# Kernel tuning notes

Hardware: AMD Instinct MI355X
Metric: run time of the kernel (lower is better)

Reference implementation:

```python
import jax, jax.numpy as jnp
import numpy as np

IOU_THRESHOLD = 0.5
EPS = 1e-7


def _make_boxes(key, n, h, w):
    k1, k2, k3, k4 = jax.random.split(key, 4)
    x1 = jax.random.uniform(k1, (n,)) * (w - 120.0)
    y1 = jax.random.uniform(k2, (n,)) * (h - 120.0)
    x2 = x1 + 20.0 + jax.random.uniform(k3, (n,)) * 100.0
    y2 = y1 + 20.0 + jax.random.uniform(k4, (n,)) * 100.0
    return jnp.stack([x1, y1, x2, y2], axis=1).astype(jnp.float32)


def setup_inputs() -> dict:
    key = jax.random.key(0)
    kd, ka, km, kt = jax.random.split(key, 4)
    N, K, H, W, MH, MW = 512, 100, 800, 800, 28, 28
    detections = _make_boxes(kd, N, H, W)[None]          # (1, N, 4) pixel coords
    annotations = _make_boxes(ka, K, H, W)[None]          # (1, K, 4) pixel coords
    masks = jax.random.uniform(km, (1, N, MH, MW, K), dtype=jnp.float32)
    masks_target = jax.random.uniform(kt, (1, K, H, W), dtype=jnp.float32)
    return {"detections": detections, "masks": masks,
            "annotations": annotations, "masks_target": masks_target}


def _overlap(a, b):
    # a: (N,4), b: (K,4) -> IoU (N,K)
    area = (b[:, 2] - b[:, 0]) * (b[:, 3] - b[:, 1])                      # (K,)
    iw = jnp.minimum(a[:, 2:3], b[None, :, 2]) - jnp.maximum(a[:, 0:1], b[None, :, 0])
    ih = jnp.minimum(a[:, 3:4], b[None, :, 3]) - jnp.maximum(a[:, 1:2], b[None, :, 1])
    iw = jnp.maximum(iw, 0.0)
    ih = jnp.maximum(ih, 0.0)
    inter = iw * ih
    ua = ((a[:, 2] - a[:, 0]) * (a[:, 3] - a[:, 1]))[:, None] + area[None, :] - inter
    return inter / jnp.maximum(ua, EPS)


def _crop_and_resize(images, boxes, box_ind, crop_size):
    # TF crop_and_resize (bilinear, extrapolation_value=0) on single-channel images.
    # images: (B, H, W); boxes: (M,4) normalized [y1,x1,y2,x2]; box_ind: (M,) int
    H, W = images.shape[1], images.shape[2]
    ch, cw = crop_size
    y1, x1, y2, x2 = boxes[:, 0], boxes[:, 1], boxes[:, 2], boxes[:, 3]
    gy = jnp.arange(ch, dtype=boxes.dtype) / (ch - 1)
    gx = jnp.arange(cw, dtype=boxes.dtype) / (cw - 1)
    in_y = (y1[:, None] + (y2 - y1)[:, None] * gy) * (H - 1)  # (M, ch)
    in_x = (x1[:, None] + (x2 - x1)[:, None] * gx) * (W - 1)  # (M, cw)
    valid_y = (in_y >= 0) & (in_y <= H - 1)
    valid_x = (in_x >= 0) & (in_x <= W - 1)
    y0 = jnp.floor(in_y)
    x0 = jnp.floor(in_x)
    yf = (in_y - y0)[:, :, None]
    xf = (in_x - x0)[:, None, :]
    y0i = jnp.clip(y0.astype(jnp.int32), 0, H - 1)
    y1i = jnp.clip(y0i + 1, 0, H - 1)
    x0i = jnp.clip(x0.astype(jnp.int32), 0, W - 1)
    x1i = jnp.clip(x0i + 1, 0, W - 1)
    b = box_ind[:, None, None]
    v00 = images[b, y0i[:, :, None], x0i[:, None, :]]
    v01 = images[b, y0i[:, :, None], x1i[:, None, :]]
    v10 = images[b, y1i[:, :, None], x0i[:, None, :]]
    v11 = images[b, y1i[:, :, None], x1i[:, None, :]]
    top = v00 + (v01 - v00) * xf
    bot = v10 + (v11 - v10) * xf
    out = top + (bot - top) * yf                                # (M, ch, cw)
    return jnp.where(valid_y[:, :, None] & valid_x[:, None, :], out, 0.0)


def reference(detections, masks, annotations, masks_target):
    d = detections[0]          # (N, 4)
    m = masks[0]               # (N, mh, mw, C)
    a = annotations[0]         # (K, 4)
    mt = masks_target[0]       # (K, H, W)
    N, mh, mw = m.shape[0], m.shape[1], m.shape[2]
    H, W = mt.shape[1], mt.shape[2]

    iou = _overlap(d, a)                               # (N, K)
    argmax_inds = jnp.argmax(iou, axis=1)              # (N,)
    max_iou = jnp.max(iou, axis=1)                     # (N,)
    valid = (max_iou >= IOU_THRESHOLD).astype(d.dtype)  # mask instead of dynamic gather

    x1, y1, x2, y2 = d[:, 0], d[:, 1], d[:, 2], d[:, 3]
    boxes = jnp.stack([y1 / H, x1 / W, y2 / H, x2 / W], axis=1)  # (N,4) normalized

    target = _crop_and_resize(mt, boxes, argmax_inds, (mh, mw))  # (N, mh, mw)
    # select the mask channel matching the assigned annotation index
    m_sel = jnp.take_along_axis(m, argmax_inds[:, None, None, None], axis=3)[..., 0]

    diff = jnp.abs(m_sel - target) * valid[:, None, None]
    n_sel = jnp.sum(valid)
    divisor = jnp.maximum(n_sel * mh * mw, 1.0)
    return jnp.sum(diff) / divisor
```

## Files before the change

### kernel.cpp

```cpp
#include <hip/hip_runtime.h>
#include <math.h>

#define N_DET 512
#define K_ANN 100
#define MH    28
#define MW    28
#define NPIX  (MH * MW)
#define IMH   800
#define IMW   800
#define IOU_THRESH 0.5f
#define EPS_F 1e-7f


__global__ __launch_bounds__(256) void maskloss_fused(
    const float* __restrict__ det,
    const float* __restrict__ masks,
    const float* __restrict__ ann,
    const float* __restrict__ mt,
    int*   __restrict__ wsi,
    float* __restrict__ wsf,
    float* __restrict__ out)
{
    __shared__ float s_iou;
    __shared__ int   s_k;
    __shared__ float wsum[4];

    const int n   = blockIdx.x;
    const int tid = threadIdx.x;

    const float dx1 = det[n * 4 + 0];
    const float dy1 = det[n * 4 + 1];
    const float dx2 = det[n * 4 + 2];
    const float dy2 = det[n * 4 + 3];

    if (tid < 64) {
        const float darea = (dx2 - dx1) * (dy2 - dy1);
        float best = -1.0f;
        int   bidx = 0x7FFFFFFF;
        for (int k = tid; k < K_ANN; k += 64) {
            const float ax1 = ann[k * 4 + 0];
            const float ay1 = ann[k * 4 + 1];
            const float ax2 = ann[k * 4 + 2];
            const float ay2 = ann[k * 4 + 3];
            const float area_k = (ax2 - ax1) * (ay2 - ay1);
            float iw = fminf(dx2, ax2) - fmaxf(dx1, ax1);
            float ih = fminf(dy2, ay2) - fmaxf(dy1, ay1);
            iw = fmaxf(iw, 0.0f);
            ih = fmaxf(ih, 0.0f);
            const float inter = iw * ih;
            const float ua = darea + area_k - inter;
            const float iou = inter / fmaxf(ua, EPS_F);
            if (iou > best) { best = iou; bidx = k; }
        }
        for (int m = 32; m > 0; m >>= 1) {
            const float ov = __shfl_xor(best, m);
            const int   oi = __shfl_xor(bidx, m);
            if (ov > best || (ov == best && oi < bidx)) { best = ov; bidx = oi; }
        }
        if (tid == 0) { s_iou = best; s_k = bidx; }
    }
    __syncthreads();

    const bool valid = (s_iou >= IOU_THRESH);
    const int  k     = s_k;

    if (valid) {
        const float by1 = dy1 / (float)IMH;
        const float bx1 = dx1 / (float)IMW;
        const float by2 = dy2 / (float)IMH;
        const float bx2 = dx2 / (float)IMW;

        const float* __restrict__ img = mt    + (size_t)k * (IMH * IMW);
        const float* __restrict__ msk = masks + (size_t)n * (NPIX * K_ANN) + k;

        auto px = [&](int p) -> float {
            const int i = p / MW;
            const int j = p - i * MW;
            const float gy = (float)i * (1.0f / (float)(MH - 1));
            const float gx = (float)j * (1.0f / (float)(MW - 1));
            const float in_y = (by1 + (by2 - by1) * gy) * (float)(IMH - 1);
            const float in_x = (bx1 + (bx2 - bx1) * gx) * (float)(IMW - 1);
            const bool vy = (in_y >= 0.0f) && (in_y <= (float)(IMH - 1));
            const bool vx = (in_x >= 0.0f) && (in_x <= (float)(IMW - 1));
            const float y0f = floorf(in_y);
            const float x0f = floorf(in_x);
            const float yf = in_y - y0f;
            const float xf = in_x - x0f;
            int y0i = (int)y0f;
            int x0i = (int)x0f;
            y0i = min(max(y0i, 0), IMH - 1);
            x0i = min(max(x0i, 0), IMW - 1);
            const int y1i = min(y0i + 1, IMH - 1);
            const int x1i = min(x0i + 1, IMW - 1);

            const float msel = msk[(size_t)p * K_ANN];
            const float v00 = img[y0i * IMW + x0i];
            const float v01 = img[y0i * IMW + x1i];
            const float v10 = img[y1i * IMW + x0i];
            const float v11 = img[y1i * IMW + x1i];
            const float top = v00 + (v01 - v00) * xf;
            const float bot = v10 + (v11 - v10) * xf;
            float outv = top + (bot - top) * yf;
            outv = (vy && vx) ? outv : 0.0f;
            return fabsf(msel - outv);
        };

        float local = px(tid) + px(tid + 256) + px(tid + 512);
        if (tid < 16) local += px(tid + 768);

        for (int off = 32; off > 0; off >>= 1)
            local += __shfl_down(local, off);
        const int wave = tid >> 6;
        const int lane = tid & 63;
        if (lane == 0) wsum[wave] = local;
        __syncthreads();
        if (tid == 0) {
            atomicAdd(&wsf[1], (wsum[0] + wsum[1]) + (wsum[2] + wsum[3]));
            atomicAdd(&wsi[0], 1);
        }
    }

    __threadfence();
    if (tid == 0) {
        if (atomicAdd(&wsi[2], 1) == N_DET - 1) {
            const int   c = atomicAdd(&wsi[0], 0);
            const float s = atomicAdd(&wsf[1], 0.0f);
            out[0] = s / fmaxf((float)c * (float)NPIX, 1.0f);
        }
    }
}

extern "C" void kernel_launch(void* const* d_in, const int* in_sizes, int n_in,
                              void* d_out, int out_size, void* d_ws, size_t ws_size,
                              hipStream_t stream) {
    const float* det   = (const float*)d_in[0];
    const float* masks = (const float*)d_in[1];
    const float* ann   = (const float*)d_in[2];
    const float* mt    = (const float*)d_in[3];
    float* out = (float*)d_out;
    int*   wsi = (int*)d_ws;
    float* wsf = (float*)d_ws;

    hipMemsetAsync(d_ws, 0, 3 * sizeof(int), stream);

    maskloss_fused<<<N_DET, 256, 0, stream>>>(det, masks, ann, mt, wsi, wsf, out);
}
```

Before: 403.5 us.

## Split each detection across eight blocks to raise parallelism

```diff
diff --git a/kernel.cpp b/kernel.cpp
--- a/kernel.cpp
+++ b/kernel.cpp
@@ -11,8 +11,13 @@
 #define IOU_THRESH 0.5f
 #define EPS_F 1e-7f
 
+#define BLK_PER_DET 8
+#define THREADS     128
+#define PX_PER_BLK  98
+#define GRID        (N_DET * BLK_PER_DET)
 
-__global__ __launch_bounds__(256) void maskloss_fused(
+
+__global__ __launch_bounds__(THREADS) void maskloss_fused(
     const float* __restrict__ det,
     const float* __restrict__ masks,
     const float* __restrict__ ann,
@@ -23,28 +28,25 @@
 {
     __shared__ float s_iou;
     __shared__ int   s_k;
-    __shared__ float wsum[4];
+    __shared__ float wsum[2];
 
-    const int n   = blockIdx.x;
+    const int b   = blockIdx.x;
+    const int n   = b >> 3;
+    const int sub = b & 7;
     const int tid = threadIdx.x;
 
-    const float dx1 = det[n * 4 + 0];
-    const float dy1 = det[n * 4 + 1];
-    const float dx2 = det[n * 4 + 2];
-    const float dy2 = det[n * 4 + 3];
+    const float4 d4 = ((const float4*)det)[n];
+    const float dx1 = d4.x, dy1 = d4.y, dx2 = d4.z, dy2 = d4.w;
 
     if (tid < 64) {
         const float darea = (dx2 - dx1) * (dy2 - dy1);
         float best = -1.0f;
         int   bidx = 0x7FFFFFFF;
         for (int k = tid; k < K_ANN; k += 64) {
-            const float ax1 = ann[k * 4 + 0];
-            const float ay1 = ann[k * 4 + 1];
-            const float ax2 = ann[k * 4 + 2];
-            const float ay2 = ann[k * 4 + 3];
-            const float area_k = (ax2 - ax1) * (ay2 - ay1);
-            float iw = fminf(dx2, ax2) - fmaxf(dx1, ax1);
-            float ih = fminf(dy2, ay2) - fmaxf(dy1, ay1);
+            const float4 a4 = ((const float4*)ann)[k];
+            const float area_k = (a4.z - a4.x) * (a4.w - a4.y);
+            float iw = fminf(dx2, a4.z) - fmaxf(dx1, a4.x);
+            float ih = fminf(dy2, a4.w) - fmaxf(dy1, a4.y);
             iw = fmaxf(iw, 0.0f);
             ih = fmaxf(ih, 0.0f);
             const float inter = iw * ih;
@@ -73,7 +75,9 @@
         const float* __restrict__ img = mt    + (size_t)k * (IMH * IMW);
         const float* __restrict__ msk = masks + (size_t)n * (NPIX * K_ANN) + k;
 
-        auto px = [&](int p) -> float {
+        float local = 0.0f;
+        if (tid < PX_PER_BLK) {
+            const int p = sub * PX_PER_BLK + tid;
             const int i = p / MW;
             const int j = p - i * MW;
             const float gy = (float)i * (1.0f / (float)(MH - 1));
@@ -102,11 +106,8 @@
             const float bot = v10 + (v11 - v10) * xf;
             float outv = top + (bot - top) * yf;
             outv = (vy && vx) ? outv : 0.0f;
-            return fabsf(msel - outv);
-        };
-
-        float local = px(tid) + px(tid + 256) + px(tid + 512);
-        if (tid < 16) local += px(tid + 768);
+            local = fabsf(msel - outv);
+        }
 
         for (int off = 32; off > 0; off >>= 1)
             local += __shfl_down(local, off);
@@ -115,14 +116,14 @@
         if (lane == 0) wsum[wave] = local;
         __syncthreads();
         if (tid == 0) {
-            atomicAdd(&wsf[1], (wsum[0] + wsum[1]) + (wsum[2] + wsum[3]));
-            atomicAdd(&wsi[0], 1);
+            atomicAdd(&wsf[1], wsum[0] + wsum[1]);
+            if (sub == 0) atomicAdd(&wsi[0], 1);
         }
     }
 
     __threadfence();
     if (tid == 0) {
-        if (atomicAdd(&wsi[2], 1) == N_DET - 1) {
+        if (atomicAdd(&wsi[2], 1) == GRID - 1) {
             const int   c = atomicAdd(&wsi[0], 0);
             const float s = atomicAdd(&wsf[1], 0.0f);
             out[0] = s / fmaxf((float)c * (float)NPIX, 1.0f);
@@ -143,5 +144,5 @@
 
     hipMemsetAsync(d_ws, 0, 3 * sizeof(int), stream);
 
-    maskloss_fused<<<N_DET, 256, 0, stream>>>(det, masks, ann, mt, wsi, wsf, out);
+    maskloss_fused<<<GRID, THREADS, 0, stream>>>(det, masks, ann, mt, wsi, wsf, out);
 }
```

Result: slower. 487.4 us (+20.8%).
